# Kernel optimization log

Measured on AMD Instinct MI355X. Metric: run time of the kernel, lower is better.

Reference implementation:

```python
import jax, jax.numpy as jnp
import numpy as np

N, E, D, H1, H2 = 50000, 800000, 128, 128, 128


def setup_inputs() -> dict:
    key = jax.random.key(0)
    ks = jax.random.split(key, 9)
    s = 0.05
    return {
        "x": jax.random.normal(ks[0], (N, D), dtype=jnp.float32),
        "edge_index": jax.random.randint(ks[1], (2, E), 0, N, dtype=jnp.int64),
        "W_l1": jax.random.normal(ks[2], (D, H1), dtype=jnp.float32) * s,
        "b_l1": jnp.zeros((H1,), dtype=jnp.float32),
        "W_r1": jax.random.normal(ks[3], (D, H1), dtype=jnp.float32) * s,
        "W_l2": jax.random.normal(ks[4], (H1, H2), dtype=jnp.float32) * s,
        "b_l2": jnp.zeros((H2,), dtype=jnp.float32),
        "W_r2": jax.random.normal(ks[5], (H1, H2), dtype=jnp.float32) * s,
        "W_e": jax.random.normal(ks[6], (2 * H2, 1), dtype=jnp.float32) * s,
        "b_e": jnp.zeros((1,), dtype=jnp.float32),
    }


def _sage_conv(h, src, tgt, n_nodes, W_l, b_l, W_r):
    # PyG SAGEConv (mean aggr): out = lin_l(mean_{j in N(i)} h_j) + lin_r(h_i)
    msg = h[src]                                              # [E, F] gather
    agg = jax.ops.segment_sum(msg, tgt, num_segments=n_nodes)  # [N, F]
    cnt = jax.ops.segment_sum(jnp.ones((src.shape[0], 1), h.dtype), tgt,
                              num_segments=n_nodes)            # [N, 1]
    mean = agg / jnp.maximum(cnt, 1.0)                         # empty nbrs -> 0
    return mean @ W_l + b_l + h @ W_r


def reference(x, edge_index, W_l1, b_l1, W_r1, W_l2, b_l2, W_r2, W_e, b_e):
    src, tgt = edge_index[0], edge_index[1]
    n_nodes = x.shape[0]
    h = jax.nn.relu(_sage_conv(x, src, tgt, n_nodes, W_l1, b_l1, W_r1))
    # dropout is identity in eval mode
    h = _sage_conv(h, src, tgt, n_nodes, W_l2, b_l2, W_r2)
    z = jnp.concatenate([h[src], h[tgt]], axis=-1)  # [E, 2*H2]
    y = z @ W_e + b_e                                # [E, 1]
    return jax.nn.sigmoid(y)
```

## Files before the change

kernel.cpp:

```cpp
#include <hip/hip_runtime.h>

#define NN 50000
#define NE 800000
#define DD 128
#define BUCKETS 196
#define PB 4096
#define PBLK 196
#define EMAX 6144
#define BPAD 264
#define PACKB 3125
#define WTB 128

typedef unsigned int uint_t;
typedef unsigned long long ull_t;
typedef unsigned short ush_t;
typedef __attribute__((ext_vector_type(8))) short short8;
typedef __attribute__((ext_vector_type(4))) float f32x4;

__device__ __forceinline__ float bflo(uint_t u) { return __uint_as_float(u << 16); }
__device__ __forceinline__ float bfhi(uint_t u) { return __uint_as_float(u & 0xffff0000u); }
__device__ __forceinline__ ush_t f2bf(float f) {
  uint_t u = __float_as_uint(f);
  u += 0x7fffu + ((u >> 16) & 1u);
  return (ush_t)(u >> 16);
}
__device__ __forceinline__ uint_t pack2(float a, float b) {
  return (uint_t)f2bf(a) | ((uint_t)f2bf(b) << 16);
}

__device__ __forceinline__ int ld_idx(const void* ei, int is64, long long i) {
  return is64 ? (int)((const long long*)ei)[i] : ((const int*)ei)[i];
}

__device__ __forceinline__ int detect64(const void* ei) {
  const unsigned long long* p = (const unsigned long long*)ei;
  unsigned long long w = p[threadIdx.x & 63];
  return __ballot((w >> 32) != 0) == 0ull ? 1 : 0;
}

__device__ __forceinline__ int block_incl_scan(int v, int tid, int* wsum) {
  int lane = tid & 63, wave = tid >> 6;
  int s = v;
#pragma unroll
  for (int off = 1; off < 64; off <<= 1) {
    int u = __shfl_up(s, off, 64);
    if (lane >= off) s += u;
  }
  if (lane == 63) wsum[wave] = s;
  __syncthreads();
  int base = 0;
  if (wave > 0) base += wsum[0];
  if (wave > 1) base += wsum[1];
  if (wave > 2) base += wsum[2];
  return base + s;
}

__global__ __launch_bounds__(256) void prep_part_k(
    const void* __restrict__ ei, int* __restrict__ bcur,
    uint_t* __restrict__ pbuf, uint_t* __restrict__ epk) {
  __shared__ int hist[256];
  __shared__ int basel[256];
  __shared__ int cur[256];
  __shared__ int gbase[256];
  __shared__ int wsum[4];
  __shared__ uint_t buf[PB];
  __shared__ unsigned char bbuf[PB];
  int tid = threadIdx.x;
  int blk = blockIdx.x;
  int is64 = detect64(ei);
  hist[tid] = 0;
  __syncthreads();
  long long base = (long long)blk * PB;
  uint_t pv[PB / 256];
#pragma unroll
  for (int i = 0; i < PB / 256; ++i) {
    long long e = base + i * 256 + tid;
    if (e < NE) {
      int s = ld_idx(ei, is64, e);
      int d = ld_idx(ei, is64, (long long)NE + e);
      pv[i] = ((uint_t)(d >> 8) << 24) | ((uint_t)(d & 255) << 16) | (uint_t)s;
      epk[e] = ((uint_t)d << 16) | (uint_t)s;
      atomicAdd(&hist[d >> 8], 1);
    } else {
      pv[i] = 0xFFFFFFFFu;
    }
  }
  __syncthreads();
  int hv = hist[tid];
  int incl = block_incl_scan(hv, tid, wsum);
  basel[tid] = incl - hv;
  cur[tid] = incl - hv;
  if (hv > 0) gbase[tid] = atomicAdd(&bcur[tid], hv);
  __syncthreads();
#pragma unroll
  for (int i = 0; i < PB / 256; ++i) {
    uint_t p = pv[i];
    if (p != 0xFFFFFFFFu) {
      int b = p >> 24;
      int r = atomicAdd(&cur[b], 1);
      buf[r] = p & 0xFFFFFFu;
      bbuf[r] = (unsigned char)b;
    }
  }
  __syncthreads();
  int total = basel[255] + hist[255];
  for (int j = tid; j < total; j += 256) {
    int b = bbuf[j];
    int slot = gbase[b] + (j - basel[b]);
    if (slot < EMAX) pbuf[(size_t)b * EMAX + slot] = buf[j];
  }
}

__global__ __launch_bounds__(256) void csr_k(
    const uint_t* __restrict__ pbuf, const int* __restrict__ bcur,
    int* __restrict__ offsets, ush_t* __restrict__ srclist,
    const float* __restrict__ x, ush_t* __restrict__ xbc,
    const float* __restrict__ Wl1, const float* __restrict__ Wr1,
    const float* __restrict__ Wl2, const float* __restrict__ Wr2,
    const float* __restrict__ We, const float* __restrict__ bl2,
    const float* __restrict__ be,
    ush_t* __restrict__ Wt1, float* __restrict__ uv, float* __restrict__ cc) {
  __shared__ int cnt[256];
  __shared__ int scur[256];
  __shared__ int wsum[4];
  __shared__ int sgb, scnt, stot;
  __shared__ uint_t ebuf[EMAX];
  int tid = threadIdx.x;
  int b = blockIdx.x;
  if (b >= BUCKETS) {
    int blk2 = b - BUCKETS;
    if (blk2 < 2) {
      const float* W = blk2 ? Wr2 : Wl2;
      int base = blk2 * 256;
      int wave = tid >> 6, lane = tid & 63;
      float e0 = We[lane], e1 = We[64 + lane];
      float f0 = We[128 + lane], f1 = We[192 + lane];
      for (int k = wave * 32; k < wave * 32 + 32; ++k) {
        float m0 = W[k * DD + lane];
        float m1 = W[k * DD + 64 + lane];
        float p = m0 * e0 + m1 * e1;
        float q = m0 * f0 + m1 * f1;
#pragma unroll
        for (int off = 32; off > 0; off >>= 1) {
          p += __shfl_down(p, off, 64);
          q += __shfl_down(q, off, 64);
        }
        if (lane == 0) {
          uv[base + k] = p;
          uv[base + 128 + k] = q;
        }
      }
      return;
    }
    if (blk2 == 2) {
      if (tid < 64) {
        int k = tid;
        float p = bl2[k] * (We[k] + We[128 + k]) +
                  bl2[k + 64] * (We[k + 64] + We[192 + k]);
#pragma unroll
        for (int off = 32; off > 0; off >>= 1) p += __shfl_down(p, off, 64);
        if (k == 0) cc[0] = p + be[0];
      }
      return;
    }
    blk2 -= 3;
    if (blk2 < PACKB) {
      int i = blk2 * 256 + tid;
      int node = i >> 4;
      int g = i & 15;
      const float4* xp = reinterpret_cast<const float4*>(x) + (size_t)i * 2;
      float4 v0 = xp[0];
      float4 v1 = xp[1];
      uint_t oa = pack2(v0.x, v0.y);
      uint_t ob = pack2(v0.z, v0.w);
      uint_t oc = pack2(v1.x, v1.y);
      uint_t od = pack2(v1.z, v1.w);
      int chunk = g >> 1;
      int off16 = (g & 1) * 8;
      ull_t* dst = reinterpret_cast<ull_t*>(
          xbc + ((size_t)chunk * NN + node) * 16 + off16);
      __builtin_nontemporal_store(((ull_t)ob << 32) | oa, dst);
      __builtin_nontemporal_store(((ull_t)od << 32) | oc, dst + 1);
      return;
    }
    blk2 -= PACKB;
    int e = blk2 * 256 + tid;
    int col = e >> 8;
    int k = e & 255;
    float v = (k < DD) ? Wl1[k * DD + col] : Wr1[(k - DD) * DD + col];
    Wt1[col * 256 + k] = f2bf(v);
    return;
  }
  int v = 0;
  if (tid < BUCKETS) {
    v = bcur[tid];
    if (v > EMAX) v = EMAX;
  }
  int incl = block_incl_scan(v, tid, wsum);
  if (tid == b) { sgb = incl - v; scnt = v; }
  if (tid == BUCKETS - 1) stot = incl;
  cnt[tid] = 0;
  __syncthreads();
  int gb = sgb;
  int ecnt = scnt;
  for (int j = tid; j < ecnt; j += 256) {
    uint_t e = pbuf[(size_t)b * EMAX + j];
    ebuf[j] = e;
    atomicAdd(&cnt[(e >> 16) & 255], 1);
  }
  __syncthreads();
  int c = cnt[tid];
  int incl2 = block_incl_scan(c, tid, wsum);
  int ex = incl2 - c;
  scur[tid] = ex;
  int node = b * 256 + tid;
  if (node < NN) offsets[node] = gb + ex;
  if (b == BUCKETS - 1 && tid == 0) offsets[NN] = stot;
  __syncthreads();
  for (int j = tid; j < ecnt; j += 256) {
    uint_t e = ebuf[j];
    int p = atomicAdd(&scur[(e >> 16) & 255], 1);
    srclist[gb + p] = (ush_t)(e & 0xFFFFu);
  }
}

__global__ __launch_bounds__(256) void agg_k(const ush_t* __restrict__ xbc,
                                             const ush_t* __restrict__ srclist,
                                             const int* __restrict__ offsets,
                                             ush_t* __restrict__ meanb) {
  int bid = blockIdx.x;
  int chunk = bid & 7;
  int grp = bid >> 3;
  int tid = threadIdx.x;
  int node = grp * 64 + (tid >> 2);
  if (node >= NN) return;
  int l4 = tid & 3;
  int lane = tid & 63;
  int lb = lane & 60;
  const ush_t* base = xbc + (size_t)chunk * NN * 16 + l4 * 4;
  int beg = offsets[node];
  int end = offsets[node + 1];
  float a0 = 0.f, a1 = 0.f, a2 = 0.f, a3 = 0.f;
  for (int c = beg; c < end; c += 16) {
    int m = end - c;
    int i0 = c + l4, i1 = c + 4 + l4, i2 = c + 8 + l4, i3 = c + 12 + l4;
    int s0 = (i0 < end) ? (int)srclist[i0] : 0;
    int s1 = (i1 < end) ? (int)srclist[i1] : 0;
    int s2 = (i2 < end) ? (int)srclist[i2] : 0;
    int s3 = (i3 < end) ? (int)srclist[i3] : 0;
    uint2 v[16];
#pragma unroll
    for (int j = 0; j < 4; ++j)
      v[j] = *reinterpret_cast<const uint2*>(base + (size_t)__shfl(s0, lb + j, 64) * 16);
#pragma unroll
    for (int j = 0; j < 4; ++j)
      v[4 + j] = *reinterpret_cast<const uint2*>(base + (size_t)__shfl(s1, lb + j, 64) * 16);
#pragma unroll
    for (int j = 0; j < 4; ++j)
      v[8 + j] = *reinterpret_cast<const uint2*>(base + (size_t)__shfl(s2, lb + j, 64) * 16);
#pragma unroll
    for (int j = 0; j < 4; ++j)
      v[12 + j] = *reinterpret_cast<const uint2*>(base + (size_t)__shfl(s3, lb + j, 64) * 16);
#pragma unroll
    for (int j = 0; j < 16; ++j) {
      if (j < m) {
        a0 += bflo(v[j].x); a1 += bfhi(v[j].x);
        a2 += bflo(v[j].y); a3 += bfhi(v[j].y);
      }
    }
  }
  float inv = 1.0f / fmaxf((float)(end - beg), 1.0f);
  uint_t o0 = pack2(a0 * inv, a1 * inv);
  uint_t o1 = pack2(a2 * inv, a3 * inv);
  __builtin_nontemporal_store(
      ((ull_t)o1 << 32) | o0,
      reinterpret_cast<ull_t*>(meanb + (size_t)node * DD + chunk * 16 + l4 * 4));
}

__global__ __launch_bounds__(256, 2) void sage_l1(
    const ush_t* __restrict__ meanb, const ush_t* __restrict__ xbc,
    const ush_t* __restrict__ Wt1, const float* __restrict__ bl,
    const float* __restrict__ uv, float2* __restrict__ t12,
    float2* __restrict__ r12) {
  __shared__ ush_t sB[128 * BPAD];
  int tid = threadIdx.x;
  int lane = tid & 63;
  int wave = tid >> 6;
  int n15 = lane & 15, quad = lane >> 4;
  int nb = blockIdx.x * 64;
#pragma unroll
  for (int it = 0; it < 16; ++it) {
    int i = it * 256 + tid;
    int col = i >> 5, c = i & 31;
    *reinterpret_cast<short8*>(&sB[col * BPAD + c * 8]) =
        reinterpret_cast<const short8*>(Wt1)[i];
  }
  __syncthreads();
  int row = nb + wave * 16 + n15;
  int arow = (row < NN) ? row : (NN - 1);
  const ush_t* a0 = meanb + (size_t)arow * DD;
  f32x4 acc[8];
#pragma unroll
  for (int t = 0; t < 8; ++t) acc[t] = (f32x4){0.f, 0.f, 0.f, 0.f};
#pragma unroll
  for (int c = 0; c < 8; ++c) {
    short8 af;
    if (c < 4) {
      af = *reinterpret_cast<const short8*>(a0 + c * 32 + quad * 8);
    } else {
      int fb = (c - 4) * 32 + quad * 8;
      af = *reinterpret_cast<const short8*>(
          xbc + ((size_t)(fb >> 4) * NN + arow) * 16 + (fb & 15));
    }
    int kb = c * 32 + quad * 8;
#pragma unroll
    for (int t = 0; t < 8; ++t) {
      short8 bf = *reinterpret_cast<const short8*>(&sB[(t * 16 + n15) * BPAD + kb]);
      acc[t] = __builtin_amdgcn_mfma_f32_16x16x32_bf16(af, bf, acc[t], 0, 0, 0);
    }
  }
  float p1[4] = {0.f, 0.f, 0.f, 0.f};
  float p2[4] = {0.f, 0.f, 0.f, 0.f};
  float q1[4] = {0.f, 0.f, 0.f, 0.f};
  float q2[4] = {0.f, 0.f, 0.f, 0.f};
#pragma unroll
  for (int t = 0; t < 8; ++t) {
    int col = t * 16 + n15;
    float b = bl[col];
    float U1 = uv[col];
    float U2 = uv[128 + col];
    float V1 = uv[256 + col];
    float V2 = uv[384 + col];
#pragma unroll
    for (int reg = 0; reg < 4; ++reg) {
      float h = fmaxf(acc[t][reg] + b, 0.f);
      p1[reg] += h * U1;
      p2[reg] += h * U2;
      q1[reg] += h * V1;
      q2[reg] += h * V2;
    }
  }
#pragma unroll
  for (int reg = 0; reg < 4; ++reg) {
    float a1 = p1[reg], a2 = p2[reg], b1 = q1[reg], b2 = q2[reg];
    for (int off = 8; off > 0; off >>= 1) {
      a1 += __shfl_down(a1, off, 16);
      a2 += __shfl_down(a2, off, 16);
      b1 += __shfl_down(b1, off, 16);
      b2 += __shfl_down(b2, off, 16);
    }
    int r = nb + wave * 16 + quad * 4 + reg;
    if (n15 == 0 && r < NN) {
      t12[r] = make_float2(a1, a2);
      r12[r] = make_float2(b1, b2);
    }
  }
}

__global__ __launch_bounds__(256) void agg2s_k(const float2* __restrict__ t12,
                                               const ush_t* __restrict__ srclist,
                                               const int* __restrict__ offsets,
                                               const float2* __restrict__ r12,
                                               float2* __restrict__ s12) {
  int t = blockIdx.x * 256 + threadIdx.x;
  int node = t >> 4;
  int lane = t & 15;
  int beg = offsets[node];
  int end = offsets[node + 1];
  float sx = 0.f, sy = 0.f;
  for (int c = beg + lane; c < end; c += 16) {
    int s = srclist[c];
    float2 v = t12[s];
    sx += v.x;
    sy += v.y;
  }
  for (int off = 8; off > 0; off >>= 1) {
    sx += __shfl_down(sx, off, 16);
    sy += __shfl_down(sy, off, 16);
  }
  if (lane == 0) {
    float inv = 1.0f / fmaxf((float)(end - beg), 1.0f);
    float2 r = r12[node];
    s12[node] = make_float2(sx * inv + r.x, sy * inv + r.y);
  }
}

__global__ __launch_bounds__(256) void edge_k(const uint_t* __restrict__ epk,
                                              const float2* __restrict__ s12,
                                              const float* __restrict__ cc,
                                              float* __restrict__ out) {
  int e = blockIdx.x * 256 + threadIdx.x;
  uint_t p = epk[e];
  float2 a = s12[p & 0xFFFFu];
  float2 b = s12[p >> 16];
  float v = a.x + b.y + cc[0];
  out[e] = 1.0f / (1.0f + __expf(-v));
}

extern "C" void kernel_launch(void* const* d_in, const int* in_sizes, int n_in,
                              void* d_out, int out_size, void* d_ws, size_t ws_size,
                              hipStream_t stream) {
  const float* x   = (const float*)d_in[0];
  const void*  ei  = d_in[1];
  const float* Wl1 = (const float*)d_in[2];
  const float* bl1 = (const float*)d_in[3];
  const float* Wr1 = (const float*)d_in[4];
  const float* Wl2 = (const float*)d_in[5];
  const float* bl2 = (const float*)d_in[6];
  const float* Wr2 = (const float*)d_in[7];
  const float* We  = (const float*)d_in[8];
  const float* be  = (const float*)d_in[9];
  float* out = (float*)d_out;

  int* bcur       = (int*)d_ws;
  int* offsets    = bcur + 256;
  uint_t* epk     = (uint_t*)(offsets + 50004);
  uint_t* pbuf    = epk + NE;
  ush_t* srclist  = (ush_t*)(pbuf + (size_t)BUCKETS * EMAX);
  ush_t* xbc      = srclist + NE;
  ush_t* meanb    = xbc + (size_t)NN * DD;
  float2* t12     = (float2*)(meanb + (size_t)NN * DD);
  float2* r12     = t12 + NN;
  float2* s12     = r12 + NN;
  ush_t* Wt1      = (ush_t*)(s12 + NN);
  float* uv       = (float*)(Wt1 + 32768);
  float* cc       = uv + 512;

  hipMemsetAsync(bcur, 0, 256 * sizeof(int), stream);
  prep_part_k<<<PBLK, 256, 0, stream>>>(ei, bcur, pbuf, epk);

  csr_k<<<BUCKETS + 3 + PACKB + WTB, 256, 0, stream>>>(
      pbuf, bcur, offsets, srclist, x, xbc, Wl1, Wr1, Wl2, Wr2, We, bl2, be,
      Wt1, uv, cc);

  agg_k<<<((NN + 63) / 64) * 8, 256, 0, stream>>>(xbc, srclist, offsets, meanb);

  sage_l1<<<(NN + 63) / 64, 256, 0, stream>>>(meanb, xbc, Wt1, bl1, uv, t12, r12);

  agg2s_k<<<(NN * 16) / 256, 256, 0, stream>>>(t12, srclist, offsets, r12, s12);

  edge_k<<<NE / 256, 256, 0, stream>>>(epk, s12, cc, out);
}
```

Before: 195.0 us.

## Widen bf16 feature chunks to 64 bytes and use 16-byte gathers in aggregation

```diff
diff --git a/kernel.cpp b/kernel.cpp
--- a/kernel.cpp
+++ b/kernel.cpp
@@ -175,10 +175,10 @@
       uint_t ob = pack2(v0.z, v0.w);
       uint_t oc = pack2(v1.x, v1.y);
       uint_t od = pack2(v1.z, v1.w);
-      int chunk = g >> 1;
-      int off16 = (g & 1) * 8;
+      int chunk = g >> 2;
+      int off32 = (g & 3) * 8;
       ull_t* dst = reinterpret_cast<ull_t*>(
-          xbc + ((size_t)chunk * NN + node) * 16 + off16);
+          xbc + ((size_t)chunk * NN + node) * 32 + off32);
       __builtin_nontemporal_store(((ull_t)ob << 32) | oa, dst);
       __builtin_nontemporal_store(((ull_t)od << 32) | oc, dst + 1);
       return;
@@ -224,57 +224,68 @@
   }
 }
 
+#define ACC8(v)                                                  \
+  a0 += bflo((v).x); a1 += bfhi((v).x); a2 += bflo((v).y);       \
+  a3 += bfhi((v).y); a4 += bflo((v).z); a5 += bfhi((v).z);       \
+  a6 += bflo((v).w); a7 += bfhi((v).w);
+
 __global__ __launch_bounds__(256) void agg_k(const ush_t* __restrict__ xbc,
                                              const ush_t* __restrict__ srclist,
                                              const int* __restrict__ offsets,
                                              ush_t* __restrict__ meanb) {
   int bid = blockIdx.x;
-  int chunk = bid & 7;
-  int grp = bid >> 3;
+  int chunk = bid & 3;
+  int grp = bid >> 2;
   int tid = threadIdx.x;
   int node = grp * 64 + (tid >> 2);
   if (node >= NN) return;
   int l4 = tid & 3;
-  int lane = tid & 63;
-  int lb = lane & 60;
-  const ush_t* base = xbc + (size_t)chunk * NN * 16 + l4 * 4;
+  const ush_t* cb = xbc + (size_t)chunk * NN * 32;
+  int loff = l4 * 8;
   int beg = offsets[node];
   int end = offsets[node + 1];
   float a0 = 0.f, a1 = 0.f, a2 = 0.f, a3 = 0.f;
-  for (int c = beg; c < end; c += 16) {
+  float a4 = 0.f, a5 = 0.f, a6 = 0.f, a7 = 0.f;
+  for (int c = beg; c < end; c += 8) {
+    int last = end - 1;
+    int ia = c + l4;      ia = ia < last ? ia : last;
+    int ib = c + 4 + l4;  ib = ib < last ? ib : last;
+    int sa = (int)__builtin_nontemporal_load(srclist + ia);
+    int sb = (int)__builtin_nontemporal_load(srclist + ib);
+    int t0 = __builtin_amdgcn_mov_dpp(sa, 0x00, 0xf, 0xf, false);
+    int t1 = __builtin_amdgcn_mov_dpp(sa, 0x55, 0xf, 0xf, false);
+    int t2 = __builtin_amdgcn_mov_dpp(sa, 0xAA, 0xf, 0xf, false);
+    int t3 = __builtin_amdgcn_mov_dpp(sa, 0xFF, 0xf, 0xf, false);
+    int t4 = __builtin_amdgcn_mov_dpp(sb, 0x00, 0xf, 0xf, false);
+    int t5 = __builtin_amdgcn_mov_dpp(sb, 0x55, 0xf, 0xf, false);
+    int t6 = __builtin_amdgcn_mov_dpp(sb, 0xAA, 0xf, 0xf, false);
+    int t7 = __builtin_amdgcn_mov_dpp(sb, 0xFF, 0xf, 0xf, false);
+    uint4 v0 = *reinterpret_cast<const uint4*>(cb + ((t0 << 5) + loff));
+    uint4 v1 = *reinterpret_cast<const uint4*>(cb + ((t1 << 5) + loff));
+    uint4 v2 = *reinterpret_cast<const uint4*>(cb + ((t2 << 5) + loff));
+    uint4 v3 = *reinterpret_cast<const uint4*>(cb + ((t3 << 5) + loff));
+    uint4 v4 = *reinterpret_cast<const uint4*>(cb + ((t4 << 5) + loff));
+    uint4 v5 = *reinterpret_cast<const uint4*>(cb + ((t5 << 5) + loff));
+    uint4 v6 = *reinterpret_cast<const uint4*>(cb + ((t6 << 5) + loff));
+    uint4 v7 = *reinterpret_cast<const uint4*>(cb + ((t7 << 5) + loff));
     int m = end - c;
-    int i0 = c + l4, i1 = c + 4 + l4, i2 = c + 8 + l4, i3 = c + 12 + l4;
-    int s0 = (i0 < end) ? (int)srclist[i0] : 0;
-    int s1 = (i1 < end) ? (int)srclist[i1] : 0;
-    int s2 = (i2 < end) ? (int)srclist[i2] : 0;
-    int s3 = (i3 < end) ? (int)srclist[i3] : 0;
-    uint2 v[16];
-#pragma unroll
-    for (int j = 0; j < 4; ++j)
-      v[j] = *reinterpret_cast<const uint2*>(base + (size_t)__shfl(s0, lb + j, 64) * 16);
-#pragma unroll
-    for (int j = 0; j < 4; ++j)
-      v[4 + j] = *reinterpret_cast<const uint2*>(base + (size_t)__shfl(s1, lb + j, 64) * 16);
-#pragma unroll
-    for (int j = 0; j < 4; ++j)
-      v[8 + j] = *reinterpret_cast<const uint2*>(base + (size_t)__shfl(s2, lb + j, 64) * 16);
-#pragma unroll
-    for (int j = 0; j < 4; ++j)
-      v[12 + j] = *reinterpret_cast<const uint2*>(base + (size_t)__shfl(s3, lb + j, 64) * 16);
-#pragma unroll
-    for (int j = 0; j < 16; ++j) {
-      if (j < m) {
-        a0 += bflo(v[j].x); a1 += bfhi(v[j].x);
-        a2 += bflo(v[j].y); a3 += bfhi(v[j].y);
-      }
-    }
+    ACC8(v0);
+    if (m > 1) { ACC8(v1); }
+    if (m > 2) { ACC8(v2); }
+    if (m > 3) { ACC8(v3); }
+    if (m > 4) { ACC8(v4); }
+    if (m > 5) { ACC8(v5); }
+    if (m > 6) { ACC8(v6); }
+    if (m > 7) { ACC8(v7); }
   }
   float inv = 1.0f / fmaxf((float)(end - beg), 1.0f);
   uint_t o0 = pack2(a0 * inv, a1 * inv);
   uint_t o1 = pack2(a2 * inv, a3 * inv);
-  __builtin_nontemporal_store(
-      ((ull_t)o1 << 32) | o0,
-      reinterpret_cast<ull_t*>(meanb + (size_t)node * DD + chunk * 16 + l4 * 4));
+  uint_t o2 = pack2(a4 * inv, a5 * inv);
+  uint_t o3 = pack2(a6 * inv, a7 * inv);
+  ull_t* dst = reinterpret_cast<ull_t*>(meanb + (size_t)node * DD + chunk * 32 + loff);
+  __builtin_nontemporal_store(((ull_t)o1 << 32) | o0, dst);
+  __builtin_nontemporal_store(((ull_t)o3 << 32) | o2, dst + 1);
 }
 
 __global__ __launch_bounds__(256, 2) void sage_l1(
@@ -308,9 +319,8 @@
     if (c < 4) {
       af = *reinterpret_cast<const short8*>(a0 + c * 32 + quad * 8);
     } else {
-      int fb = (c - 4) * 32 + quad * 8;
       af = *reinterpret_cast<const short8*>(
-          xbc + ((size_t)(fb >> 4) * NN + arow) * 16 + (fb & 15));
+          xbc + ((size_t)(c - 4) * NN + arow) * 32 + quad * 8);
     }
     int kb = c * 32 + quad * 8;
 #pragma unroll
@@ -433,7 +443,7 @@
       pbuf, bcur, offsets, srclist, x, xbc, Wl1, Wr1, Wl2, Wr2, We, bl2, be,
       Wt1, uv, cc);
 
-  agg_k<<<((NN + 63) / 64) * 8, 256, 0, stream>>>(xbc, srclist, offsets, meanb);
+  agg_k<<<((NN + 63) / 64) * 4, 256, 0, stream>>>(xbc, srclist, offsets, meanb);
 
   sage_l1<<<(NN + 63) / 64, 256, 0, stream>>>(meanb, xbc, Wt1, bl1, uv, t12, r12);
 
```

After: 194.8 us. About the same (-0.1%).
